# Kernel optimization log

Measured on AMD Instinct MI355X. Metric: run time of the kernel, lower is better.

The kernel has to match this reference:

```python
import jax, jax.numpy as jnp
import numpy as np

HIDDEN = 4096
N_HEADS = 32
N_KV_HEADS = 8
HEAD_DIM = 128
N_GROUPS = N_HEADS // N_KV_HEADS
ROPE_THETA = 10000.0
QMAX = 127.0
B, S = 1, 2048


def setup_inputs() -> dict:
    key = jax.random.key(0)
    ks = jax.random.split(key, 5)
    hidden_states = jax.random.normal(ks[0], (B, S, HIDDEN), dtype=jnp.float32)
    # additive causal mask (Llama style: 0 on/below diagonal, large negative above)
    tril = jnp.tril(jnp.ones((S, S), dtype=bool))
    attention_mask = jnp.where(tril, 0.0, -1e9).astype(jnp.float32)[None, None]
    position_ids = jnp.arange(S, dtype=jnp.int64 if jax.config.jax_enable_x64 else jnp.int32)[None].astype(jnp.int32)
    sc = 1.0 / np.sqrt(HIDDEN)
    wq = jax.random.normal(ks[1], (HIDDEN, N_HEADS * HEAD_DIM), dtype=jnp.float32) * sc
    wk = jax.random.normal(ks[2], (HIDDEN, N_KV_HEADS * HEAD_DIM), dtype=jnp.float32) * sc
    wv = jax.random.normal(ks[3], (HIDDEN, N_KV_HEADS * HEAD_DIM), dtype=jnp.float32) * sc
    wo = jax.random.normal(ks[4], (N_HEADS * HEAD_DIM, HIDDEN), dtype=jnp.float32) * sc
    return {"hidden_states": hidden_states, "attention_mask": attention_mask,
            "position_ids": position_ids, "wq": wq, "wk": wk, "wv": wv, "wo": wo}


def _rope_cos_sin(position_ids):
    # [B, S, HEAD_DIM]
    inv_freq = 1.0 / (ROPE_THETA ** (jnp.arange(0, HEAD_DIM, 2, dtype=jnp.float32) / HEAD_DIM))
    freqs = position_ids.astype(jnp.float32)[..., None] * inv_freq  # [B,S,HEAD_DIM//2]
    emb = jnp.concatenate([freqs, freqs], axis=-1)
    return jnp.cos(emb), jnp.sin(emb)


def _rotate_half(x):
    x1, x2 = jnp.split(x, 2, axis=-1)
    return jnp.concatenate([-x2, x1], axis=-1)


def _fake_quant(x):
    scale = jnp.max(jnp.abs(x)) / QMAX  # global absmax
    return jnp.round(x / scale) * scale


def reference(hidden_states, attention_mask, position_ids, wq, wk, wv, wo):
    bsz, q_len, _ = hidden_states.shape
    q = (hidden_states @ wq).reshape(bsz, q_len, N_HEADS, HEAD_DIM).transpose(0, 2, 1, 3)
    k = (hidden_states @ wk).reshape(bsz, q_len, N_KV_HEADS, HEAD_DIM).transpose(0, 2, 1, 3)
    v = (hidden_states @ wv).reshape(bsz, q_len, N_KV_HEADS, HEAD_DIM).transpose(0, 2, 1, 3)

    cos, sin = _rope_cos_sin(position_ids)  # [B,S,D]
    cos, sin = cos[:, None], sin[:, None]   # broadcast over heads
    q = q * cos + _rotate_half(q) * sin
    k = k * cos + _rotate_half(k) * sin

    # repeat_kv: [B, Hkv, S, D] -> [B, H, S, D]
    k = jnp.repeat(k, N_GROUPS, axis=1)
    v = jnp.repeat(v, N_GROUPS, axis=1)

    # fake quant: global absmax round-trip on Q, K, V
    q = _fake_quant(q)
    k = _fake_quant(k)
    v = _fake_quant(v)

    scores = jnp.einsum('bhqd,bhkd->bhqk', q, k) / np.sqrt(HEAD_DIM)
    scores = scores + attention_mask
    probs = jax.nn.softmax(scores.astype(jnp.float32), axis=-1).astype(q.dtype)
    attn = jnp.einsum('bhqk,bhkd->bhqd', probs, v)
    attn = attn.transpose(0, 2, 1, 3).reshape(bsz, q_len, N_HEADS * HEAD_DIM)
    return attn @ wo
```

## Files before the change

kernel.cpp:

```cpp
#include <hip/hip_runtime.h>
#include <math.h>

#define S_LEN 2048
#define HID 4096
#define NH 32
#define NKV 8
#define HD 128
#define NQKV 6144

typedef __bf16 bf16x8 __attribute__((ext_vector_type(8)));
typedef float f32x4 __attribute__((ext_vector_type(4)));
typedef short short8v __attribute__((ext_vector_type(8)));

__device__ inline short f2bf(float f) {
  union { float f; unsigned u; } a; a.f = f;
  unsigned r = a.u + 0x7fffu + ((a.u >> 16) & 1u);
  return (short)(r >> 16);
}

__device__ inline void glds16(const void* g, void* l) {
  __builtin_amdgcn_global_load_lds((const __attribute__((address_space(1))) void*)g,
                                   (__attribute__((address_space(3))) void*)l, 16, 0, 0);
}

template <int CTRL>
__device__ inline float dpp_max_step(float x) {
  int y = __builtin_amdgcn_update_dpp(0, __float_as_int(x), CTRL, 0xf, 0xf, false);
  return fmaxf(x, __int_as_float(y));
}

__global__ __launch_bounds__(256) void cast_h(const float* __restrict__ X,
                                              short* __restrict__ Y, int n4) {
  int i = blockIdx.x * 256 + threadIdx.x;
  if (i >= n4) return;
  float4 v = ((const float4*)X)[i];
  short4 o;
  o.x = f2bf(v.x); o.y = f2bf(v.y); o.z = f2bf(v.z); o.w = f2bf(v.w);
  ((short4*)Y)[i] = o;
}

__global__ __launch_bounds__(256) void cast_wt(const float* __restrict__ W,
                                               short* __restrict__ Wt, int Ncols) {
  __shared__ float t[32][33];
  int n0 = blockIdx.x * 32, k0 = blockIdx.y * 32;
  int tx = threadIdx.x, ty = threadIdx.y;
  for (int j = 0; j < 4; j++)
    t[ty + 8 * j][tx] = W[(size_t)(k0 + ty + 8 * j) * Ncols + n0 + tx];
  __syncthreads();
  for (int j = 0; j < 4; j++)
    Wt[(size_t)(n0 + ty + 8 * j) * 4096 + k0 + tx] = f2bf(t[tx][ty + 8 * j]);
}

__global__ void rope_table(const int* __restrict__ pos_ids, float* __restrict__ tc,
                           float* __restrict__ ts) {
  int p = blockIdx.x, i = threadIdx.x;
  float pos = (float)pos_ids[p];
  float inv = powf(10000.0f, -((float)(2 * i)) * (1.0f / 128.0f));
  float a = pos * inv;
  tc[p * 64 + i] = cosf(a);
  ts[p * 64 + i] = sinf(a);
}

__global__ __launch_bounds__(256) void rope_absmax(float* __restrict__ C,
                                                   const float* __restrict__ tc,
                                                   const float* __restrict__ ts,
                                                   unsigned* __restrict__ scal) {
  __shared__ float lc[64], lsn[64];
  __shared__ float red[3][4];
  const int p = blockIdx.x, t = threadIdx.x;
  if (t < 64) { lc[t] = tc[p * 64 + t]; lsn[t] = ts[p * 64 + t]; }
  __syncthreads();
  float* row = C + (size_t)p * NQKV;
  float mq = 0.f, mk = 0.f, mv = 0.f;
#pragma unroll
  for (int j = 0; j < 8; j++) {
    int idx = t + 256 * j;
    int i = idx & 63, col = (idx >> 6) * 128 + i;
    float c = lc[i], s = lsn[i];
    float x1 = row[col], x2 = row[col + 64];
    float y1 = x1 * c - x2 * s, y2 = x2 * c + x1 * s;
    row[col] = y1; row[col + 64] = y2;
    mq = fmaxf(mq, fmaxf(fabsf(y1), fabsf(y2)));
  }
#pragma unroll
  for (int j = 0; j < 2; j++) {
    int idx = t + 256 * j;
    int i = idx & 63, col = 4096 + (idx >> 6) * 128 + i;
    float c = lc[i], s = lsn[i];
    float x1 = row[col], x2 = row[col + 64];
    float y1 = x1 * c - x2 * s, y2 = x2 * c + x1 * s;
    row[col] = y1; row[col + 64] = y2;
    mk = fmaxf(mk, fmaxf(fabsf(y1), fabsf(y2)));
  }
#pragma unroll
  for (int j = 0; j < 4; j++) {
    float v = row[5120 + t + 256 * j];
    mv = fmaxf(mv, fabsf(v));
  }
  for (int off = 32; off; off >>= 1) {
    mq = fmaxf(mq, __shfl_xor(mq, off, 64));
    mk = fmaxf(mk, __shfl_xor(mk, off, 64));
    mv = fmaxf(mv, __shfl_xor(mv, off, 64));
  }
  const int wave = t >> 6;
  if ((t & 63) == 0) { red[0][wave] = mq; red[1][wave] = mk; red[2][wave] = mv; }
  __syncthreads();
  if (t < 3) {
    float m = fmaxf(fmaxf(red[t][0], red[t][1]), fmaxf(red[t][2], red[t][3]));
    atomicMax(scal + t, __float_as_uint(m));
  }
}

__global__ __launch_bounds__(256) void quant_q(const float* __restrict__ C,
                                               const unsigned* __restrict__ scal,
                                               short* __restrict__ Qi) {
  int idx = blockIdx.x * 256 + threadIdx.x;
  float scale = __uint_as_float(scal[0]) * (1.0f / 127.0f);
  int p = idx >> 12, c = idx & 4095;
  Qi[idx] = f2bf(rintf(C[(size_t)p * NQKV + c] / scale));
}

__global__ __launch_bounds__(256) void quant_k(const float* __restrict__ C,
                                               const unsigned* __restrict__ scal,
                                               short* __restrict__ Ki) {
  int idx = blockIdx.x * 256 + threadIdx.x;
  float scale = __uint_as_float(scal[1]) * (1.0f / 127.0f);
  int h = idx >> 18, p = (idx >> 7) & 2047, d = idx & 127;
  Ki[idx] = f2bf(rintf(C[(size_t)p * NQKV + 4096 + h * 128 + d] / scale));
}

__global__ __launch_bounds__(256) void quant_vt(const float* __restrict__ C,
                                                const unsigned* __restrict__ scal,
                                                short* __restrict__ Vt) {
  __shared__ float t[64][65];
  int h = blockIdx.x, pt = blockIdx.y, dt = blockIdx.z;
  float scale = __uint_as_float(scal[2]) * (1.0f / 127.0f);
  int tid = threadIdx.x;
  for (int j = 0; j < 16; j++) {
    int q = tid + 256 * j;
    int pl = q >> 6, dl = q & 63;
    t[dl][pl] = C[(size_t)(pt * 64 + pl) * NQKV + 5120 + h * 128 + dt * 64 + dl];
  }
  __syncthreads();
  for (int j = 0; j < 16; j++) {
    int q = tid + 256 * j;
    int dl = q >> 6, pl = q & 63;
    Vt[(size_t)(h * 128 + dt * 64 + dl) * 2048 + pt * 64 + pl] =
        f2bf(rintf(t[dl][pl] / scale));
  }
}

__global__ __launch_bounds__(256, 2) void gemm_bt(const short* __restrict__ A, int lda,
                                                  const short* __restrict__ B,
                                                  float* __restrict__ C, int ldc, int K) {
  __shared__ alignas(16) short As[2][4096];
  __shared__ alignas(16) short Bs[2][4096];
  const int tid = threadIdx.x;
  const int wave = tid >> 6, lane = tid & 63;
  const int quad = lane >> 4, l15 = lane & 15;
  const int m0 = blockIdx.y * 128, n0 = blockIdx.x * 128;
  const int wm = (wave >> 1) * 64, wn = (wave & 1) * 64;
  f32x4 acc[4][4] = {};
  const int sr = wave * 16 + (lane >> 2);
  const int sg = (lane & 3) * 8;
  const short* Ag0 = A + (size_t)(m0 + sr) * lda + sg;
  const short* Ag1 = A + (size_t)(m0 + 64 + sr) * lda + sg;
  const short* Bg0 = B + (size_t)(n0 + sr) * K + sg;
  const short* Bg1 = B + (size_t)(n0 + 64 + sr) * K + sg;
  auto stage = [&](int kk, int b) {
    glds16(Ag0 + kk, &As[b][wave * 512]);
    glds16(Ag1 + kk, &As[b][2048 + wave * 512]);
    glds16(Bg0 + kk, &Bs[b][wave * 512]);
    glds16(Bg1 + kk, &Bs[b][2048 + wave * 512]);
  };
  stage(0, 0);
  int b = 0;
  for (int k0 = 0; k0 < K; k0 += 32) {
    __syncthreads();
    const int nk = (k0 + 32 < K) ? k0 + 32 : k0;
    stage(nk, b ^ 1);
    bf16x8 af[4], bfr[4];
#pragma unroll
    for (int t = 0; t < 4; t++) {
      af[t] = *(const bf16x8*)&As[b][(wm + t * 16 + l15) * 32 + quad * 8];
      bfr[t] = *(const bf16x8*)&Bs[b][(wn + t * 16 + l15) * 32 + quad * 8];
    }
#pragma unroll
    for (int tm = 0; tm < 4; tm++)
#pragma unroll
      for (int tn = 0; tn < 4; tn++)
        acc[tm][tn] =
            __builtin_amdgcn_mfma_f32_16x16x32_bf16(af[tm], bfr[tn], acc[tm][tn], 0, 0, 0);
    b ^= 1;
  }
#pragma unroll
  for (int tm = 0; tm < 4; tm++)
#pragma unroll
    for (int tn = 0; tn < 4; tn++) {
      const int row = m0 + wm + tm * 16 + quad * 4;
      const int col = n0 + wn + tn * 16 + l15;
#pragma unroll
      for (int r = 0; r < 4; r++) C[(size_t)(row + r) * ldc + col] = acc[tm][tn][r];
    }
}

__global__ __launch_bounds__(512, 2) void gemm_bt8(const short* __restrict__ A, int lda,
                                                   const short* __restrict__ B, int ldb,
                                                   float* __restrict__ C, int ldc, int K) {
  __shared__ alignas(16) short As[2][16384];
  __shared__ alignas(16) short Bs[2][16384];
  const int tid = threadIdx.x;
  const int wave = tid >> 6, lane = tid & 63;
  const int quad = lane >> 4, l15 = lane & 15;
  const int wm = wave >> 2, wn = wave & 3;
  const int m0 = blockIdx.y * 256, n0 = blockIdx.x * 256;

  const int rsub = lane >> 3;
  const int csw = (lane & 7) ^ rsub;
  size_t asrc[4], bsrc[4];
#pragma unroll
  for (int s = 0; s < 4; s++) {
    int row = s * 64 + wave * 8 + rsub;
    asrc[s] = (size_t)(m0 + row) * lda + csw * 8;
    bsrc[s] = (size_t)(n0 + row) * ldb + csw * 8;
  }
  const int nt = K >> 6;

  auto stA = [&](int t2, int s) {
    const int kk = (t2 < nt ? t2 : nt - 1) << 6;
    glds16(A + asrc[s] + kk, &As[t2 & 1][(s * 64 + wave * 8) * 64]);
  };
  auto stB = [&](int t2, int s) {
    const int kk = (t2 < nt ? t2 : nt - 1) << 6;
    glds16(B + bsrc[s] + kk, &Bs[t2 & 1][(s * 64 + wave * 8) * 64]);
  };

  int swq[2];
#pragma unroll
  for (int kc = 0; kc < 2; kc++)
    swq[kc] = l15 * 64 + (((kc * 4 + quad) ^ (l15 & 7)) * 8);

  f32x4 acc[8][4] = {};

  stB(0, 0); stB(0, 1); stB(0, 2); stB(0, 3);
  stA(0, 0); stA(0, 2); stA(0, 1); stA(0, 3);
  asm volatile("s_waitcnt vmcnt(2)" ::: "memory");
  __builtin_amdgcn_s_barrier();

  for (int t = 0; t < nt; t++) {
    const short* Ab = As[t & 1];
    const short* Bb = Bs[t & 1];
    bf16x8 bfr[4][2];
#pragma unroll
    for (int p = 0; p < 4; p++) {
      if (p == 0) {
#pragma unroll
        for (int n = 0; n < 4; n++)
#pragma unroll
          for (int kc = 0; kc < 2; kc++)
            bfr[n][kc] = *(const bf16x8*)&Bb[(wn * 64 + n * 16) * 64 + swq[kc]];
      }
      bf16x8 a0k0 = *(const bf16x8*)&Ab[(wm * 128 + (2 * p) * 16) * 64 + swq[0]];
      bf16x8 a0k1 = *(const bf16x8*)&Ab[(wm * 128 + (2 * p) * 16) * 64 + swq[1]];
      bf16x8 a1k0 = *(const bf16x8*)&Ab[(wm * 128 + (2 * p + 1) * 16) * 64 + swq[0]];
      bf16x8 a1k1 = *(const bf16x8*)&Ab[(wm * 128 + (2 * p + 1) * 16) * 64 + swq[1]];
      if (p == 0) { stB(t + 1, 0); stB(t + 1, 1); }
      if (p == 1) { stB(t + 1, 2); stB(t + 1, 3); }
      if (p == 2) { stA(t + 1, 0); stA(t + 1, 2); }
      if (p == 3) { stA(t + 1, 1); stA(t + 1, 3); }
      __builtin_amdgcn_s_barrier();
      __builtin_amdgcn_s_setprio(1);
#pragma unroll
      for (int n = 0; n < 4; n++) {
        acc[2 * p][n] =
            __builtin_amdgcn_mfma_f32_16x16x32_bf16(a0k0, bfr[n][0], acc[2 * p][n], 0, 0, 0);
        acc[2 * p][n] =
            __builtin_amdgcn_mfma_f32_16x16x32_bf16(a0k1, bfr[n][1], acc[2 * p][n], 0, 0, 0);
        acc[2 * p + 1][n] = __builtin_amdgcn_mfma_f32_16x16x32_bf16(a1k0, bfr[n][0],
                                                                    acc[2 * p + 1][n], 0, 0, 0);
        acc[2 * p + 1][n] = __builtin_amdgcn_mfma_f32_16x16x32_bf16(a1k1, bfr[n][1],
                                                                    acc[2 * p + 1][n], 0, 0, 0);
      }
      __builtin_amdgcn_s_setprio(0);
      if (p == 1) asm volatile("s_waitcnt vmcnt(4)" ::: "memory");
      if (p == 3) asm volatile("s_waitcnt vmcnt(2)" ::: "memory");
      __builtin_amdgcn_s_barrier();
    }
  }
#pragma unroll
  for (int m = 0; m < 8; m++)
#pragma unroll
    for (int n = 0; n < 4; n++) {
      const int row = m0 + wm * 128 + m * 16 + quad * 4;
      const int col = n0 + wn * 64 + n * 16 + l15;
#pragma unroll
      for (int r = 0; r < 4; r++) C[(size_t)(row + r) * ldc + col] = acc[m][n][r];
    }
}

__global__ __launch_bounds__(256, 2) void attn_fused(const short* __restrict__ Qi,
                                                     const short* __restrict__ Ki,
                                                     const short* __restrict__ Vt,
                                                     const unsigned* __restrict__ scal,
                                                     short* __restrict__ Oa) {
  __shared__ alignas(16) short Ks[2][64 * 128];
  __shared__ alignas(16) short Vs[2][128 * 64];
  __shared__ alignas(16) short Ps[4][16 * 72];
  const int tid = threadIdx.x;
  const int wave = tid >> 6, lane = tid & 63;
  const int quad = lane >> 4, l15 = lane & 15;
  const int swz = l15 & 7;
  const int h = blockIdx.x & 31, pq = blockIdx.x >> 5;
  const int kvh = h >> 2;
  const float qs = __uint_as_float(scal[0]) * (1.0f / 127.0f);
  const float ksc = __uint_as_float(scal[1]) * (1.0f / 127.0f);
  const float vsc = __uint_as_float(scal[2]) * (1.0f / 127.0f);
  const float sscale = qs * ksc * 0.08838834764831845f * 1.4426950408889634f;
  const short* Kg = Ki + (size_t)kvh * S_LEN * HD;
  const short* Vg = Vt + (size_t)kvh * HD * S_LEN;

  union { short8v s; bf16x8 b; } uone;
  uone.s = short8v{0x3F80, 0x3F80, 0x3F80, 0x3F80, 0x3F80, 0x3F80, 0x3F80, 0x3F80};
  const bf16x8 vone = uone.b;

  int koff[4], voff[4];
#pragma unroll
  for (int j = 0; j < 4; j++) {
    int slot = j * 256 + tid;
    int r = slot >> 4, seg = slot & 15;
    koff[j] = r * 128 + ((seg ^ (r & 7)) * 8);
    int vr = slot >> 3, vseg = slot & 7;
    voff[j] = vr * 2048 + ((vseg ^ (vr & 7)) * 8);
  }
  auto stage = [&](int k0, int b) {
#pragma unroll
    for (int j = 0; j < 4; j++)
      glds16(Kg + (size_t)k0 * HD + koff[j], &Ks[b][(j * 256 + wave * 64) * 8]);
#pragma unroll
    for (int j = 0; j < 4; j++)
      glds16(Vg + (size_t)k0 + voff[j], &Vs[b][(j * 256 + wave * 64) * 8]);
  };

  stage(0, 0);
  int buf = 0;
  for (int ph = 0; ph < 2; ph++) {
    const int qt = ph ? 31 - pq : pq;
    const int rw = qt * 64 + wave * 16;
    bf16x8 aq[4];
#pragma unroll
    for (int kc = 0; kc < 4; kc++)
      aq[kc] = *(const bf16x8*)(Qi + (size_t)(rw + l15) * 4096 + h * 128 + kc * 32 +
                                quad * 8);
    f32x4 o[9] = {};
    float m_[4] = {-INFINITY, -INFINITY, -INFINITY, -INFINITY};
    const int nkt = qt + 1;
    for (int kt = 0; kt < nkt; kt++) {
      const int k0 = kt * 64;
      __syncthreads();
      const int nx = (kt + 1 < nkt) ? k0 + 64 : 0;
      stage(nx, buf ^ 1);

      const short* Kb = Ks[buf];
      const short* Vb = Vs[buf];
      f32x4 sf[4];
      __builtin_amdgcn_s_setprio(1);
#pragma unroll
      for (int tn = 0; tn < 4; tn++) {
        f32x4 s = {0.f, 0.f, 0.f, 0.f};
#pragma unroll
        for (int kc = 0; kc < 4; kc++) {
          bf16x8 bk = *(const bf16x8*)&Kb[(tn * 16 + l15) * 128 + ((kc * 4 + quad) ^ swz) * 8];
          s = __builtin_amdgcn_mfma_f32_16x16x32_bf16(aq[kc], bk, s, 0, 0, 0);
        }
        sf[tn] = s;
      }
      __builtin_amdgcn_s_setprio(0);

      const bool diag = (kt == qt);
#pragma unroll
      for (int r = 0; r < 4; r++) {
        const int grow = rw + quad * 4 + r;
        float mx = -3.0e38f;
        if (diag) {
#pragma unroll
          for (int tn = 0; tn < 4; tn++) {
            float v = sf[tn][r] * sscale;
            if (k0 + tn * 16 + l15 > grow) v = -3.0e38f;
            sf[tn][r] = v;
            mx = fmaxf(mx, v);
          }
        } else {
#pragma unroll
          for (int tn = 0; tn < 4; tn++) {
            float v = sf[tn][r] * sscale;
            sf[tn][r] = v;
            mx = fmaxf(mx, v);
          }
        }
        mx = dpp_max_step<0x121>(mx);
        mx = dpp_max_step<0x122>(mx);
        mx = dpp_max_step<0x124>(mx);
        mx = dpp_max_step<0x128>(mx);
        const float mo = m_[r];
        const float mn = fmaxf(mo, mx);
        m_[r] = mn;
        const float alpha = __builtin_amdgcn_exp2f(mo - mn);
#pragma unroll
        for (int tn = 0; tn < 4; tn++) {
          float p = __builtin_amdgcn_exp2f(sf[tn][r] - mn);
          Ps[wave][(quad * 4 + r) * 72 + tn * 16 + l15] =
              (short)((__float_as_uint(p) + 0x8000u) >> 16);
        }
        if (__ballot(alpha != 1.0f)) {
#pragma unroll
          for (int t = 0; t < 9; t++) o[t][r] *= alpha;
        }
      }
      __builtin_amdgcn_s_setprio(1);
#pragma unroll
      for (int kk = 0; kk < 2; kk++) {
        bf16x8 ap = *(const bf16x8*)&Ps[wave][l15 * 72 + kk * 32 + quad * 8];
#pragma unroll
        for (int tn = 0; tn < 8; tn++) {
          bf16x8 bv = *(const bf16x8*)&Vb[(tn * 16 + l15) * 64 + ((kk * 4 + quad) ^ swz) * 8];
          o[tn] = __builtin_amdgcn_mfma_f32_16x16x32_bf16(ap, bv, o[tn], 0, 0, 0);
        }
        o[8] = __builtin_amdgcn_mfma_f32_16x16x32_bf16(ap, vone, o[8], 0, 0, 0);
      }
      __builtin_amdgcn_s_setprio(0);
      buf ^= 1;
    }
#pragma unroll
    for (int r = 0; r < 4; r++) {
      const int grow = rw + quad * 4 + r;
      const float sc = vsc / o[8][r];
#pragma unroll
      for (int tn = 0; tn < 8; tn++)
        Oa[(size_t)grow * 4096 + h * 128 + tn * 16 + l15] = f2bf(o[tn][r] * sc);
    }
  }
}

extern "C" void kernel_launch(void* const* d_in, const int* in_sizes, int n_in,
                              void* d_out, int out_size, void* d_ws, size_t ws_size,
                              hipStream_t stream) {
  (void)in_sizes; (void)n_in; (void)out_size; (void)ws_size;
  const float* H  = (const float*)d_in[0];
  const int*   pos = (const int*)d_in[2];
  const float* wq = (const float*)d_in[3];
  const float* wk = (const float*)d_in[4];
  const float* wv = (const float*)d_in[5];
  const float* wo = (const float*)d_in[6];
  char* ws = (char*)d_ws;
  short* Hb   = (short*)(ws + 0);
  short* Wt   = (short*)(ws + 16777216);
  short* Wot  = (short*)(ws + 67108864);
  float* C    = (float*)(ws + 100663296);
  short* Qi   = (short*)(ws + 150994944);
  short* Ki   = (short*)(ws + 167772160);
  short* Vt   = (short*)(ws + 171966464);
  short* Oa   = (short*)(ws + 176160768);
  float* tc   = (float*)(ws + 192937984);
  float* tsn  = (float*)(ws + 193462272);
  unsigned* scal = (unsigned*)(ws + 193986560);

  hipLaunchKernelGGL(cast_h, dim3(8192), dim3(256), 0, stream, H, Hb, 2097152);
  hipLaunchKernelGGL(cast_wt, dim3(128, 128), dim3(32, 8), 0, stream, wq, Wt, 4096);
  hipLaunchKernelGGL(cast_wt, dim3(32, 128), dim3(32, 8), 0, stream, wk,
                     Wt + (size_t)4096 * 4096, 1024);
  hipLaunchKernelGGL(cast_wt, dim3(32, 128), dim3(32, 8), 0, stream, wv,
                     Wt + (size_t)5120 * 4096, 1024);
  hipLaunchKernelGGL(cast_wt, dim3(128, 128), dim3(32, 8), 0, stream, wo, Wot, 4096);
  hipLaunchKernelGGL(rope_table, dim3(2048), dim3(64), 0, stream, pos, tc, tsn);
  hipMemsetAsync(scal, 0, 16, stream);
  hipLaunchKernelGGL(gemm_bt8, dim3(24, 8), dim3(512), 0, stream, Hb, 4096, Wt, 4096, C,
                     6144, 4096);
  hipLaunchKernelGGL(rope_absmax, dim3(2048), dim3(256), 0, stream, C, tc, tsn, scal);
  hipLaunchKernelGGL(quant_q, dim3(32768), dim3(256), 0, stream, C, scal, Qi);
  hipLaunchKernelGGL(quant_k, dim3(8192), dim3(256), 0, stream, C, scal, Ki);
  hipLaunchKernelGGL(quant_vt, dim3(8, 32, 2), dim3(256), 0, stream, C, scal, Vt);
  hipLaunchKernelGGL(attn_fused, dim3(512), dim3(256), 0, stream, Qi, Ki, Vt, scal, Oa);
  hipLaunchKernelGGL(gemm_bt, dim3(32, 16), dim3(256), 0, stream, Oa, 4096, Wot,
                     (float*)d_out, 4096, 4096);
}
```

Before: 586.5 us.

## Restructure GEMM main loop: prefetch B two tiles ahead, cut barriers per k-step

The bf16 MFMA GEMM main loop is rebuilt. It now reads all B fragments once, then issues all A loads for the next tile and B loads two tiles ahead. The 8 MFMA row-blocks run back-to-back, with only two workgroup barriers per k-step instead of eight. The aim is to cut barrier and synchronisation overhead and give global-to-LDS loads more time to overlap compute. In exchange the MFMA work is less interleaved with LDS reads, and the vmcnt accounting gets tighter, which carries correctness risk if the counts are wrong.

```diff
diff --git a/kernel.cpp b/kernel.cpp
--- a/kernel.cpp
+++ b/kernel.cpp
@@ -226,13 +226,17 @@
   }
   const int nt = K >> 6;
 
-  auto stA = [&](int t2, int s) {
+  auto stA = [&](int t2) {
     const int kk = (t2 < nt ? t2 : nt - 1) << 6;
-    glds16(A + asrc[s] + kk, &As[t2 & 1][(s * 64 + wave * 8) * 64]);
+#pragma unroll
+    for (int s = 0; s < 4; s++)
+      glds16(A + asrc[s] + kk, &As[t2 & 1][(s * 64 + wave * 8) * 64]);
   };
-  auto stB = [&](int t2, int s) {
+  auto stB = [&](int t2) {
     const int kk = (t2 < nt ? t2 : nt - 1) << 6;
-    glds16(B + bsrc[s] + kk, &Bs[t2 & 1][(s * 64 + wave * 8) * 64]);
+#pragma unroll
+    for (int s = 0; s < 4; s++)
+      glds16(B + bsrc[s] + kk, &Bs[t2 & 1][(s * 64 + wave * 8) * 64]);
   };
 
   int swq[2];
@@ -242,50 +246,40 @@
 
   f32x4 acc[8][4] = {};
 
-  stB(0, 0); stB(0, 1); stB(0, 2); stB(0, 3);
-  stA(0, 0); stA(0, 2); stA(0, 1); stA(0, 3);
-  asm volatile("s_waitcnt vmcnt(2)" ::: "memory");
+  stB(0); stA(0);
+  stB(1);
+  asm volatile("s_waitcnt vmcnt(4)" ::: "memory");
   __builtin_amdgcn_s_barrier();
 
   for (int t = 0; t < nt; t++) {
     const short* Ab = As[t & 1];
     const short* Bb = Bs[t & 1];
+    stA(t + 1);
     bf16x8 bfr[4][2];
 #pragma unroll
-    for (int p = 0; p < 4; p++) {
-      if (p == 0) {
-#pragma unroll
-        for (int n = 0; n < 4; n++)
-#pragma unroll
-          for (int kc = 0; kc < 2; kc++)
-            bfr[n][kc] = *(const bf16x8*)&Bb[(wn * 64 + n * 16) * 64 + swq[kc]];
+    for (int n = 0; n < 4; n++) {
+      bfr[n][0] = *(const bf16x8*)&Bb[(wn * 64 + n * 16) * 64 + swq[0]];
+      bfr[n][1] = *(const bf16x8*)&Bb[(wn * 64 + n * 16) * 64 + swq[1]];
+    }
+    asm volatile("s_waitcnt lgkmcnt(0)" ::: "memory");
+    __builtin_amdgcn_sched_barrier(0);
+    __builtin_amdgcn_s_barrier();
+    stB(t + 2);
+    __builtin_amdgcn_s_setprio(1);
+#pragma unroll
+    for (int m = 0; m < 8; m++) {
+      bf16x8 a0 = *(const bf16x8*)&Ab[(wm * 128 + m * 16) * 64 + swq[0]];
+      bf16x8 a1 = *(const bf16x8*)&Ab[(wm * 128 + m * 16) * 64 + swq[1]];
+#pragma unroll
+      for (int n = 0; n < 4; n++) {
+        acc[m][n] = __builtin_amdgcn_mfma_f32_16x16x32_bf16(a0, bfr[n][0], acc[m][n], 0, 0, 0);
+        acc[m][n] = __builtin_amdgcn_mfma_f32_16x16x32_bf16(a1, bfr[n][1], acc[m][n], 0, 0, 0);
       }
-      bf16x8 a0k0 = *(const bf16x8*)&Ab[(wm * 128 + (2 * p) * 16) * 64 + swq[0]];
-      bf16x8 a0k1 = *(const bf16x8*)&Ab[(wm * 128 + (2 * p) * 16) * 64 + swq[1]];
-      bf16x8 a1k0 = *(const bf16x8*)&Ab[(wm * 128 + (2 * p + 1) * 16) * 64 + swq[0]];
-      bf16x8 a1k1 = *(const bf16x8*)&Ab[(wm * 128 + (2 * p + 1) * 16) * 64 + swq[1]];
-      if (p == 0) { stB(t + 1, 0); stB(t + 1, 1); }
-      if (p == 1) { stB(t + 1, 2); stB(t + 1, 3); }
-      if (p == 2) { stA(t + 1, 0); stA(t + 1, 2); }
-      if (p == 3) { stA(t + 1, 1); stA(t + 1, 3); }
-      __builtin_amdgcn_s_barrier();
-      __builtin_amdgcn_s_setprio(1);
-#pragma unroll
-      for (int n = 0; n < 4; n++) {
-        acc[2 * p][n] =
-            __builtin_amdgcn_mfma_f32_16x16x32_bf16(a0k0, bfr[n][0], acc[2 * p][n], 0, 0, 0);
-        acc[2 * p][n] =
-            __builtin_amdgcn_mfma_f32_16x16x32_bf16(a0k1, bfr[n][1], acc[2 * p][n], 0, 0, 0);
-        acc[2 * p + 1][n] = __builtin_amdgcn_mfma_f32_16x16x32_bf16(a1k0, bfr[n][0],
-                                                                    acc[2 * p + 1][n], 0, 0, 0);
-        acc[2 * p + 1][n] = __builtin_amdgcn_mfma_f32_16x16x32_bf16(a1k1, bfr[n][1],
-                                                                    acc[2 * p + 1][n], 0, 0, 0);
-      }
-      __builtin_amdgcn_s_setprio(0);
-      if (p == 1) asm volatile("s_waitcnt vmcnt(4)" ::: "memory");
-      if (p == 3) asm volatile("s_waitcnt vmcnt(2)" ::: "memory");
-      __builtin_amdgcn_s_barrier();
-    }
+    }
+    __builtin_amdgcn_s_setprio(0);
+    asm volatile("s_waitcnt vmcnt(4)" ::: "memory");
+    __builtin_amdgcn_s_barrier();
+    __builtin_amdgcn_sched_barrier(0);
   }
 #pragma unroll
   for (int m = 0; m < 8; m++)
```

Result: no change. 596.7 us (+1.7%).
